# Optimization experiments

Hardware: AMD Instinct MI355X
Metric: run time of the kernel (lower is better)

The kernel has to match this reference:

```python
import jax, jax.numpy as jnp
import numpy as np

N_NODES = 100000
N_EDGES = 3200000
D_FEAT = 512
HIDDEN = 16
N_CLASSES = 7


def setup_inputs() -> dict:
    key = jax.random.key(0)
    k1, k2, k3, k4 = jax.random.split(key, 4)
    x = jax.random.normal(k1, (N_NODES, D_FEAT), dtype=jnp.float32)
    edge_index = jax.random.randint(k2, (2, N_EDGES), 0, N_NODES, dtype=jnp.int64)
    # Glorot-ish scaled weights
    W1 = jax.random.normal(k3, (D_FEAT, HIDDEN), dtype=jnp.float32) * (1.0 / np.sqrt(D_FEAT))
    b1 = jnp.zeros((HIDDEN,), dtype=jnp.float32)
    W2 = jax.random.normal(k4, (HIDDEN, N_CLASSES), dtype=jnp.float32) * (1.0 / np.sqrt(HIDDEN))
    b2 = jnp.zeros((N_CLASSES,), dtype=jnp.float32)
    return {"x": x, "edge_index": edge_index, "W1": W1, "b1": b1, "W2": W2, "b2": b2}


def _gcn_norm(edge_index, num_nodes):
    # Add self-loops, then symmetric normalization: D^-1/2 A D^-1/2
    loop = jnp.arange(num_nodes, dtype=edge_index.dtype)
    src = jnp.concatenate([edge_index[0], loop])
    dst = jnp.concatenate([edge_index[1], loop])
    deg = jax.ops.segment_sum(jnp.ones_like(dst, dtype=jnp.float32), dst,
                              num_segments=num_nodes)
    dinv = jnp.where(deg > 0, jax.lax.rsqrt(deg), 0.0)
    w = dinv[src] * dinv[dst]  # [E+N]
    return src, dst, w


def _gcn_conv(x, W, b, src, dst, w, num_nodes):
    h = x @ W                               # transform first (small out dim)
    m = jax.ops.segment_sum(h[src] * w[:, None], dst, num_segments=num_nodes)
    return m + b


def reference(x, edge_index, W1, b1, W2, b2):
    n = x.shape[0]
    src, dst, w = _gcn_norm(edge_index, n)
    h = jax.nn.relu(_gcn_conv(x, W1, b1, src, dst, w, n))
    # dropout is identity at inference
    logits = _gcn_conv(h, W2, b2, src, dst, w, n)
    return jax.nn.log_softmax(logits, axis=1)
```

## Files before the change

kernel.cpp:

```cpp
#include <hip/hip_runtime.h>
#include <cmath>

#define N_NODES   100000
#define N_EDGES   3200000
#define D_FEAT    512
#define HIDDEN    16
#define N_CLASSES 7

#define NCHUNK 625
#define CHUNK  5120
#define NBKT   1563
#define BCAP   2560
#define GEMMB  391

typedef __attribute__((ext_vector_type(4))) float  f32x4;
typedef __attribute__((ext_vector_type(8))) short  bf16x8;

__device__ __forceinline__ short f2bf(float f) {
    union { float f; unsigned u; } v; v.f = f;
    unsigned r = v.u + 0x7fffu + ((v.u >> 16) & 1u);
    return (short)(r >> 16);
}
__device__ __forceinline__ float bf2f(unsigned short s) {
    union { unsigned u; float f; } v; v.u = ((unsigned)s) << 16;
    return v.f;
}
__device__ __forceinline__ float bflo(unsigned u) {
    union { unsigned u; float f; } v; v.u = u << 16; return v.f;
}
__device__ __forceinline__ float bfhi(unsigned u) {
    union { unsigned u; float f; } v; v.u = u & 0xFFFF0000u; return v.f;
}

__global__ __launch_bounds__(1024) void k_fused1(const int* __restrict__ src,
                                                 const int* __restrict__ dst,
                                                 unsigned* __restrict__ cnt,
                                                 unsigned* __restrict__ packed,
                                                 const float* __restrict__ x,
                                                 const float* __restrict__ w1,
                                                 float* __restrict__ graw) {
    __shared__ __align__(16) short w1t[16][520];
    __shared__ unsigned h[NBKT];
    int t = threadIdx.x;

    if (blockIdx.x < NCHUNK) {
        int b = blockIdx.x;
        for (int i = t; i < NBKT; i += 1024) h[i] = 0u;
        __syncthreads();
        int base = b * CHUNK;
        #pragma unroll
        for (int k = 0; k < 5; ++k)
            atomicAdd(&h[((unsigned)dst[base + k * 1024 + t]) >> 6], 1u);
        __syncthreads();
        for (int i = t; i < NBKT; i += 1024) {
            unsigned c = h[i];
            h[i] = c ? ((unsigned)i * BCAP + atomicAdd(&cnt[i], c)) : 0u;
        }
        __syncthreads();
        #pragma unroll
        for (int k = 0; k < 5; ++k) {
            int e = base + k * 1024 + t;
            unsigned d = (unsigned)dst[e];
            unsigned pos = atomicAdd(&h[d >> 6], 1u);
            packed[pos] = ((d & 63u) << 24) | (unsigned)src[e];
        }
    } else {
        for (int idx = t; idx < D_FEAT * HIDDEN; idx += 1024) {
            int k = idx >> 4, n = idx & 15;
            w1t[n][k] = f2bf(w1[idx]);
        }
        __syncthreads();
        int lane = t & 63, wid = t >> 6;
        int m  = lane & 15;
        int kg = lane >> 4;
        int tile = (blockIdx.x - NCHUNK) * 16 + wid;
        if (tile >= (N_NODES / 16)) return;

        const f32x4* xr = (const f32x4*)(x + (size_t)(tile * 16 + m) * D_FEAT);
        f32x4 acc = {0.f, 0.f, 0.f, 0.f};
        #pragma unroll
        for (int ks = 0; ks < 16; ++ks) {
            f32x4 x0 = xr[ks * 8 + kg * 2];
            f32x4 x1 = xr[ks * 8 + kg * 2 + 1];
            bf16x8 a;
            a[0] = f2bf(x0[0]); a[1] = f2bf(x0[1]); a[2] = f2bf(x0[2]); a[3] = f2bf(x0[3]);
            a[4] = f2bf(x1[0]); a[5] = f2bf(x1[1]); a[6] = f2bf(x1[2]); a[7] = f2bf(x1[3]);
            bf16x8 bb = *(const bf16x8*)&w1t[m][ks * 32 + kg * 8];
            acc = __builtin_amdgcn_mfma_f32_16x16x32_bf16(a, bb, acc, 0, 0, 0);
        }
        size_t base = (size_t)tile * 256;
        #pragma unroll
        for (int r = 0; r < 4; ++r)
            graw[base + (kg * 4 + r) * 16 + m] = acc[r];
    }
}

__global__ __launch_bounds__(256) void k_bucket(const unsigned* __restrict__ packed,
                                                const unsigned* __restrict__ cnt,
                                                const float* __restrict__ graw,
                                                unsigned* __restrict__ deg,
                                                unsigned* __restrict__ row_start,
                                                float* __restrict__ dinv,
                                                int* __restrict__ csr_src,
                                                unsigned short* __restrict__ h1p) {
    __shared__ unsigned hh[4][64], sc[64], cur[64];
    __shared__ float dls[64];
    int t = threadIdx.x, b = blockIdx.x;
    int w = t >> 6, l = t & 63;
    unsigned rs = (unsigned)b * BCAP;
    unsigned re = rs + cnt[b];
    hh[w][l] = 0u;
    __syncthreads();
    for (unsigned i = rs + t; i < re; i += 256)
        atomicAdd(&hh[w][packed[i] >> 24], 1u);
    __syncthreads();
    unsigned total = 0u;
    if (t < 64) {
        total = hh[0][t] + hh[1][t] + hh[2][t] + hh[3][t];
        sc[t] = total;
    }
    __syncthreads();
    #pragma unroll
    for (int off = 1; off < 64; off <<= 1) {
        unsigned add = (t >= off && t < 64) ? sc[t - off] : 0u;
        __syncthreads();
        if (t < 64) sc[t] += add;
        __syncthreads();
    }
    if (t < 64) {
        unsigned excl = sc[t] - total;
        int node = b * 64 + t;
        float di = rsqrtf((float)(total + 1u));
        dls[t] = di;
        if (node < N_NODES) {
            deg[node]       = total;
            row_start[node] = rs + excl;
            dinv[node]      = di;
        }
        cur[t] = rs + excl;
    }
    __syncthreads();
    #pragma unroll
    for (int k = 0; k < 4; ++k) {
        int i = t + k * 256;
        int node = b * 64 + (i >> 4);
        if (node < N_NODES)
            h1p[(size_t)b * 1024 + i] =
                (unsigned short)f2bf(dls[i >> 4] * graw[(size_t)b * 1024 + i]);
    }
    for (unsigned i = rs + t; i < re; i += 256) {
        unsigned p = packed[i];
        unsigned pos = atomicAdd(&cur[p >> 24], 1u);
        csr_src[pos] = (int)(p & 0xFFFFFFu);
    }
}

__global__ __launch_bounds__(256) void k_gather1(const int* __restrict__ csr_src,
                                                 const unsigned* __restrict__ row_start,
                                                 const unsigned* __restrict__ deg,
                                                 const unsigned short* __restrict__ h1p,
                                                 const float* __restrict__ dinv,
                                                 const float* __restrict__ w2,
                                                 const float* __restrict__ b1,
                                                 float* __restrict__ h2p) {
    __shared__ float w2s[16][8];
    __shared__ float b1s[16];
    int tid  = threadIdx.x;
    if (tid < 128) {
        int jj = tid >> 3, c = tid & 7;
        w2s[jj][c] = (c < N_CLASSES) ? w2[jj * N_CLASSES + c] : 0.f;
    }
    if (tid < 16) b1s[tid] = b1[tid];
    __syncthreads();

    int lane = tid & 63;
    int node = blockIdx.x * 4 + (tid >> 6);
    int half = lane & 1;
    int slot = lane >> 1;

    unsigned start = row_start[node];
    unsigned end   = start + deg[node];

    float acc[8] = {0,0,0,0,0,0,0,0};
    uint4 sv = *(const uint4*)(h1p + (size_t)node * 16 + half * 8);
    if (lane < 2) {
        acc[0] += bflo(sv.x); acc[1] += bfhi(sv.x);
        acc[2] += bflo(sv.y); acc[3] += bfhi(sv.y);
        acc[4] += bflo(sv.z); acc[5] += bfhi(sv.z);
        acc[6] += bflo(sv.w); acc[7] += bfhi(sv.w);
    }
    for (unsigned e0 = start; e0 < end; e0 += 32) {
        unsigned idx = e0 + (unsigned)slot;
        if (idx < end) {
            int s = csr_src[idx];
            uint4 rv = *(const uint4*)(h1p + (size_t)s * 16 + half * 8);
            acc[0] += bflo(rv.x); acc[1] += bfhi(rv.x);
            acc[2] += bflo(rv.y); acc[3] += bfhi(rv.y);
            acc[4] += bflo(rv.z); acc[5] += bfhi(rv.z);
            acc[6] += bflo(rv.w); acc[7] += bfhi(rv.w);
        }
    }
    #pragma unroll
    for (int mk = 2; mk <= 32; mk <<= 1) {
        #pragma unroll
        for (int k = 0; k < 8; ++k) acc[k] += __shfl_xor(acc[k], mk);
    }
    float oth[8];
    #pragma unroll
    for (int k = 0; k < 8; ++k) oth[k] = __shfl_xor(acc[k], 1);

    float di = dinv[node];
    float h[16];
    #pragma unroll
    for (int k = 0; k < 8; ++k) {
        float glo = half ? oth[k] : acc[k];
        float ghi = half ? acc[k] : oth[k];
        h[k]     = fmaxf(fmaf(di, glo, b1s[k]),     0.f);
        h[k + 8] = fmaxf(fmaf(di, ghi, b1s[k + 8]), 0.f);
    }
    int c = lane & 7;
    float o = 0.f;
    #pragma unroll
    for (int j = 0; j < 16; ++j) o = fmaf(h[j], w2s[j][c], o);
    if (lane < 8)
        h2p[(size_t)node * 8 + c] = (c < N_CLASSES) ? di * o : 0.f;
}

__global__ __launch_bounds__(256) void k_gather2(const int* __restrict__ csr_src,
                                                 const unsigned* __restrict__ row_start,
                                                 const unsigned* __restrict__ deg,
                                                 const float* __restrict__ dinv,
                                                 const float* __restrict__ h2p,
                                                 const float* __restrict__ b2,
                                                 float* __restrict__ out) {
    int tid  = threadIdx.x;
    int lane = tid & 63;
    int node = blockIdx.x * 4 + (tid >> 6);
    int half = lane & 1;
    int slot = lane >> 1;

    unsigned start = row_start[node];
    unsigned end   = start + deg[node];

    float acc[4] = {0, 0, 0, 0};
    f32x4 sv = *(const f32x4*)(h2p + (size_t)node * 8 + half * 4);
    if (lane < 2) { acc[0] += sv[0]; acc[1] += sv[1]; acc[2] += sv[2]; acc[3] += sv[3]; }
    for (unsigned e0 = start; e0 < end; e0 += 32) {
        unsigned idx = e0 + (unsigned)slot;
        if (idx < end) {
            int s = csr_src[idx];
            f32x4 rv = *(const f32x4*)(h2p + (size_t)s * 8 + half * 4);
            acc[0] += rv[0]; acc[1] += rv[1]; acc[2] += rv[2]; acc[3] += rv[3];
        }
    }
    #pragma unroll
    for (int mk = 2; mk <= 32; mk <<= 1) {
        #pragma unroll
        for (int k = 0; k < 4; ++k) acc[k] += __shfl_xor(acc[k], mk);
    }
    float oth[4];
    #pragma unroll
    for (int k = 0; k < 4; ++k) oth[k] = __shfl_xor(acc[k], 1);

    float l[8];
    #pragma unroll
    for (int k = 0; k < 4; ++k) {
        l[k]     = half ? oth[k] : acc[k];
        l[k + 4] = half ? acc[k] : oth[k];
    }
    float di = dinv[node];
    float lg[N_CLASSES];
    float mx = -1e30f;
    #pragma unroll
    for (int cc = 0; cc < N_CLASSES; ++cc) {
        lg[cc] = fmaf(di, l[cc], b2[cc]);
        mx = fmaxf(mx, lg[cc]);
    }
    float sum = 0.f;
    #pragma unroll
    for (int cc = 0; cc < N_CLASSES; ++cc) sum += __expf(lg[cc] - mx);
    float lse = mx + __logf(sum);
    if (lane < N_CLASSES) {
        float v = lg[0];
        #pragma unroll
        for (int cc = 1; cc < N_CLASSES; ++cc) if (lane == cc) v = lg[cc];
        out[(size_t)node * N_CLASSES + lane] = v - lse;
    }
}

extern "C" void kernel_launch(void* const* d_in, const int* in_sizes, int n_in,
                              void* d_out, int out_size, void* d_ws, size_t ws_size,
                              hipStream_t stream) {
    const float* x  = (const float*)d_in[0];
    const int*   ei = (const int*)d_in[1];
    const float* w1 = (const float*)d_in[2];
    const float* b1 = (const float*)d_in[3];
    const float* w2 = (const float*)d_in[4];
    const float* b2 = (const float*)d_in[5];
    float* out = (float*)d_out;

    const int* src = ei;
    const int* dst = ei + N_EDGES;

    unsigned* w32            = (unsigned*)d_ws;
    float*    dinv           = (float*)(w32 + 0);
    unsigned short* h1p      = (unsigned short*)(w32 + 102400);
    float*    h2p            = (float*)(w32 + 902400);
    unsigned* deg            = w32 + 1702400;
    unsigned* row_start      = w32 + 1804800;
    unsigned* cnt            = w32 + 1907200;
    float*    graw           = (float*)(w32 + 1909248);
    unsigned* packed         = w32 + 3509248;
    int*      csr_src        = (int*)(w32 + 7510528);

    hipMemsetAsync(cnt, 0, NBKT * sizeof(unsigned), stream);
    k_fused1 <<<NCHUNK + GEMMB, 1024, 0, stream>>>(src, dst, cnt, packed, x, w1, graw);
    k_bucket <<<NBKT,  256, 0, stream>>>(packed, cnt, graw, deg, row_start, dinv, csr_src, h1p);
    k_gather1<<<25000, 256, 0, stream>>>(csr_src, row_start, deg, h1p, dinv, w2, b1, h2p);
    k_gather2<<<25000, 256, 0, stream>>>(csr_src, row_start, deg, dinv, h2p, b2, out);
}
```

Measured before the change: 478.4 us.

## Stage bucket scatter in LDS with local prefix sum before coalesced global write

The edge-bucketing blocks now each process 20000 edges instead of 5120, sort them into buckets in shared memory using a local histogram and block-wide prefix scan, then copy each bucket contiguously to global memory with wave-wide writes. This replaces scattered per-edge global writes with coalesced bucket-run writes and cuts the number of global atomics on cnt. In exchange it uses about 100KB of shared memory per block, which limits occupancy. It also leaves only 160 scatter blocks, so those blocks get far less parallelism and take on extra scan synchronisation.

```diff
diff --git a/kernel.cpp b/kernel.cpp
--- a/kernel.cpp
+++ b/kernel.cpp
@@ -7,8 +7,8 @@
 #define HIDDEN    16
 #define N_CLASSES 7
 
-#define NCHUNK 625
-#define CHUNK  5120
+#define SBLK   160
+#define SCH    20000
 #define NBKT   1563
 #define BCAP   2560
 #define GEMMB  391
@@ -39,32 +39,71 @@
                                                  const float* __restrict__ x,
                                                  const float* __restrict__ w1,
                                                  float* __restrict__ graw) {
-    __shared__ __align__(16) short w1t[16][520];
-    __shared__ unsigned h[NBKT];
+    __shared__ __align__(16) unsigned smem[4691 + SCH];
     int t = threadIdx.x;
 
-    if (blockIdx.x < NCHUNK) {
+    if (blockIdx.x < SBLK) {
+        unsigned* hist   = smem;
+        unsigned* lstart = smem + 1563;
+        unsigned* gbase  = smem + 3127;
+        unsigned* buf    = smem + 4691;
         int b = blockIdx.x;
-        for (int i = t; i < NBKT; i += 1024) h[i] = 0u;
-        __syncthreads();
-        int base = b * CHUNK;
-        #pragma unroll
-        for (int k = 0; k < 5; ++k)
-            atomicAdd(&h[((unsigned)dst[base + k * 1024 + t]) >> 6], 1u);
+        int ebase = b * SCH;
+
+        for (int i = t; i < NBKT; i += 1024) hist[i] = 0u;
+        __syncthreads();
+        for (int k = 0; k < 20; ++k) {
+            int idx = k * 1024 + t;
+            if (idx < SCH) atomicAdd(&hist[((unsigned)dst[ebase + idx]) >> 6], 1u);
+        }
+        __syncthreads();
+        {
+            unsigned* sc = buf;
+            int i0 = t * 2;
+            unsigned a0 = (i0     < NBKT) ? hist[i0]     : 0u;
+            unsigned a1 = (i0 + 1 < NBKT) ? hist[i0 + 1] : 0u;
+            unsigned s  = a0 + a1;
+            sc[t] = s; __syncthreads();
+            #pragma unroll
+            for (int off = 1; off < 1024; off <<= 1) {
+                unsigned add = (t >= off) ? sc[t - off] : 0u;
+                __syncthreads();
+                sc[t] += add;
+                __syncthreads();
+            }
+            unsigned excl = sc[t] - s;
+            if (i0     < NBKT) lstart[i0]     = excl;
+            if (i0 + 1 < NBKT) lstart[i0 + 1] = excl + a0;
+            if (t == 0) lstart[NBKT] = (unsigned)SCH;
+        }
         __syncthreads();
         for (int i = t; i < NBKT; i += 1024) {
-            unsigned c = h[i];
-            h[i] = c ? ((unsigned)i * BCAP + atomicAdd(&cnt[i], c)) : 0u;
-        }
-        __syncthreads();
-        #pragma unroll
-        for (int k = 0; k < 5; ++k) {
-            int e = base + k * 1024 + t;
-            unsigned d = (unsigned)dst[e];
-            unsigned pos = atomicAdd(&h[d >> 6], 1u);
-            packed[pos] = ((d & 63u) << 24) | (unsigned)src[e];
+            unsigned c = hist[i];
+            gbase[i] = c ? ((unsigned)i * BCAP + atomicAdd(&cnt[i], c)) : 0u;
+        }
+        __syncthreads();
+        for (int i = t; i < NBKT; i += 1024) hist[i] = lstart[i];
+        __syncthreads();
+        for (int k = 0; k < 20; ++k) {
+            int idx = k * 1024 + t;
+            if (idx < SCH) {
+                int e = ebase + idx;
+                unsigned d = (unsigned)dst[e];
+                unsigned pos = atomicAdd(&hist[d >> 6], 1u);
+                buf[pos] = ((d & 63u) << 24) | (unsigned)src[e];
+            }
+        }
+        __syncthreads();
+        int w = t >> 6, lane = t & 63;
+        for (int i = w; i < NBKT; i += 16) {
+            unsigned ls = lstart[i];
+            unsigned c  = lstart[i + 1] - ls;
+            unsigned gb = gbase[i];
+            for (unsigned j = lane; j < c; j += 64)
+                packed[gb + j] = buf[ls + j];
         }
     } else {
+        short (*w1t)[520] = (short(*)[520])smem;
         for (int idx = t; idx < D_FEAT * HIDDEN; idx += 1024) {
             int k = idx >> 4, n = idx & 15;
             w1t[n][k] = f2bf(w1[idx]);
@@ -73,7 +112,7 @@
         int lane = t & 63, wid = t >> 6;
         int m  = lane & 15;
         int kg = lane >> 4;
-        int tile = (blockIdx.x - NCHUNK) * 16 + wid;
+        int tile = (blockIdx.x - SBLK) * 16 + wid;
         if (tile >= (N_NODES / 16)) return;
 
         const f32x4* xr = (const f32x4*)(x + (size_t)(tile * 16 + m) * D_FEAT);
@@ -314,7 +353,7 @@
     int*      csr_src        = (int*)(w32 + 7510528);
 
     hipMemsetAsync(cnt, 0, NBKT * sizeof(unsigned), stream);
-    k_fused1 <<<NCHUNK + GEMMB, 1024, 0, stream>>>(src, dst, cnt, packed, x, w1, graw);
+    k_fused1 <<<SBLK + GEMMB, 1024, 0, stream>>>(src, dst, cnt, packed, x, w1, graw);
     k_bucket <<<NBKT,  256, 0, stream>>>(packed, cnt, graw, deg, row_start, dinv, csr_src, h1p);
     k_gather1<<<25000, 256, 0, stream>>>(csr_src, row_start, deg, h1p, dinv, w2, b1, h2p);
     k_gather2<<<25000, 256, 0, stream>>>(csr_src, row_start, deg, dinv, h2p, b2, out);
```

After: 439.3 us. -8.2%, faster.
